# Kernel optimization log

Measured on AMD Instinct MI355X. Metric: run time of the kernel, lower is better.

The kernel has to match this reference:

```python
import jax, jax.numpy as jnp
import numpy as np

B, C, T, H, L = 64, 256, 1536, 512, 2


def setup_inputs() -> dict:
    key = jax.random.key(0)
    ks = jax.random.split(key, 9)
    s = 1.0 / np.sqrt(H)  # PyTorch LSTM init scale
    inp = {
        "x": jax.random.normal(ks[0], (B, C, T), dtype=jnp.float32),
        "Wih0": jax.random.uniform(ks[1], (4 * H, C), jnp.float32, -s, s),
        "Whh0": jax.random.uniform(ks[2], (4 * H, H), jnp.float32, -s, s),
        "bih0": jax.random.uniform(ks[3], (4 * H,), jnp.float32, -s, s),
        "bhh0": jax.random.uniform(ks[4], (4 * H,), jnp.float32, -s, s),
        "Wih1": jax.random.uniform(ks[5], (4 * H, H), jnp.float32, -s, s),
        "Whh1": jax.random.uniform(ks[6], (4 * H, H), jnp.float32, -s, s),
        "bih1": jax.random.uniform(ks[7], (4 * H,), jnp.float32, -s, s),
        "bhh1": jax.random.uniform(ks[8], (4 * H,), jnp.float32, -s, s),
    }
    return inp


def _lstm_layer(x_btf, Wih, Whh, bih, bhh):
    # x_btf: [B, T, F]; gates precomputed from inputs (input GEMM batched over T)
    gx = jnp.einsum("btf,gf->btg", x_btf, Wih) + bih + bhh  # [B, T, 4H]
    gx = jnp.transpose(gx, (1, 0, 2))  # [T, B, 4H] for scan over time
    h0 = jnp.zeros((x_btf.shape[0], H), x_btf.dtype)
    c0 = jnp.zeros_like(h0)

    def step(carry, g_t):
        h, c = carry
        g = g_t + h @ Whh.T  # [B, 4H]
        i, f, gg, o = jnp.split(g, 4, axis=-1)  # PyTorch gate order i,f,g,o
        i = jax.nn.sigmoid(i)
        f = jax.nn.sigmoid(f)
        gg = jnp.tanh(gg)
        o = jax.nn.sigmoid(o)
        c = f * c + i * gg
        h = o * jnp.tanh(c)
        return (h, c), h

    _, hs = jax.lax.scan(step, (h0, c0), gx)  # hs: [T, B, H]
    return jnp.transpose(hs, (1, 0, 2))  # [B, T, H]


def reference(x, Wih0, Whh0, bih0, bhh0, Wih1, Whh1, bih1, bhh1):
    # forward: permute [B, C, T] -> [B, T, C], run 2-layer LSTM, return outputs
    h = jnp.transpose(x, (0, 2, 1))
    h = _lstm_layer(h, Wih0, Whh0, bih0, bhh0)
    h = _lstm_layer(h, Wih1, Whh1, bih1, bhh1)
    return h
```

## Files before the change

kernel.cpp:

```cpp
#include <hip/hip_runtime.h>
#include <cstdint>
#include <cstddef>

#define B_SZ 64
#define T_SZ 1536
#define C_SZ 256
#define H_SZ 512
#define G4H  2048
#define POLL_BUDGET 5000000

typedef __attribute__((ext_vector_type(8))) short short8;
typedef __attribute__((ext_vector_type(4))) float f32x4;

#define AL(p) __hip_atomic_load((p), __ATOMIC_RELAXED, __HIP_MEMORY_SCOPE_AGENT)
#define AS(p, x) __hip_atomic_store((p), (x), __ATOMIC_RELAXED, __HIP_MEMORY_SCOPE_AGENT)
#define SPIN_GE(p, tgt) \
    while (AL(p) < (tgt)) { if (++polls > POLL_BUDGET) break; }

__device__ __forceinline__ unsigned short f2bf_rne(float f) {
    unsigned u = __float_as_uint(f);
    unsigned r = (u + 0x7FFF + ((u >> 16) & 1)) >> 16;
    return (unsigned short)r;
}
__device__ __forceinline__ float sigmoid_f(float x) {
    return 1.f / (1.f + __expf(-x));
}
__device__ __forceinline__ float tanh_f(float x) {
    return 1.f - 2.f / (__expf(2.f * x) + 1.f);
}

template<int AMODE>
__global__ __launch_bounds__(256)
void gemm_gx(const float* __restrict__ A, const float* __restrict__ W,
             const float* __restrict__ bias1, const float* __restrict__ bias2,
             float* __restrict__ gx, int K, int astride_b, int t0g, int tlen)
{
    __shared__ float a_s[8][132];
    __shared__ float b_s[8][132];
    const int tb = blockIdx.x, nb = blockIdx.y, b = blockIdx.z;
    const int tloc = tb * 128;
    const int tglb = t0g + tloc;
    const int r0 = nb * 128;
    const float* Ab = A + (size_t)b * astride_b;
    const int tid = threadIdx.x;
    const int tx = tid & 15, ty = tid >> 4;
    float acc[8][8] = {};

    for (int k0 = 0; k0 < K; k0 += 8) {
        if (AMODE == 0) {
            const int row = tid >> 5;
            const int col = (tid & 31) << 2;
            const float4 v = *(const float4*)(Ab + (size_t)(k0 + row) * T_SZ + tglb + col);
            *(float4*)&a_s[row][col] = v;
        } else {
            const int row  = tid >> 1;
            const int half = (tid & 1) << 2;
            const float4 v = *(const float4*)(Ab + (size_t)(tglb + row) * H_SZ + k0 + half);
            a_s[half + 0][row] = v.x; a_s[half + 1][row] = v.y;
            a_s[half + 2][row] = v.z; a_s[half + 3][row] = v.w;
        }
        {
            const int row  = tid >> 1;
            const int half = (tid & 1) << 2;
            const float4 v = *(const float4*)(W + (size_t)(r0 + row) * K + k0 + half);
            b_s[half + 0][row] = v.x; b_s[half + 1][row] = v.y;
            b_s[half + 2][row] = v.z; b_s[half + 3][row] = v.w;
        }
        __syncthreads();
        #pragma unroll
        for (int kk = 0; kk < 8; ++kk) {
            float4 a0 = *(const float4*)&a_s[kk][tx * 8];
            float4 a1 = *(const float4*)&a_s[kk][tx * 8 + 4];
            float4 w0 = *(const float4*)&b_s[kk][ty * 8];
            float4 w1 = *(const float4*)&b_s[kk][ty * 8 + 4];
            float av[8] = {a0.x, a0.y, a0.z, a0.w, a1.x, a1.y, a1.z, a1.w};
            float wv[8] = {w0.x, w0.y, w0.z, w0.w, w1.x, w1.y, w1.z, w1.w};
            #pragma unroll
            for (int i = 0; i < 8; ++i)
                #pragma unroll
                for (int j = 0; j < 8; ++j)
                    acc[i][j] += wv[i] * av[j];
        }
        __syncthreads();
    }
    float bs[8];
    #pragma unroll
    for (int i = 0; i < 8; ++i)
        bs[i] = bias1[r0 + ty * 8 + i] + bias2[r0 + ty * 8 + i];
    #pragma unroll
    for (int j = 0; j < 8; ++j) {
        float* dst = gx + ((size_t)(tloc + tx * 8 + j) * B_SZ + b) * G4H + r0 + ty * 8;
        float4 o0 = {acc[0][j] + bs[0], acc[1][j] + bs[1], acc[2][j] + bs[2], acc[3][j] + bs[3]};
        float4 o1 = {acc[4][j] + bs[4], acc[5][j] + bs[5], acc[6][j] + bs[6], acc[7][j] + bs[7]};
        *(float4*)dst = o0; *(float4*)(dst + 4) = o1;
    }
}

__global__ void wsplit(const float* __restrict__ w,
                       unsigned short* __restrict__ hi,
                       unsigned short* __restrict__ lo, int n)
{
    const int i = blockIdx.x * 256 + threadIdx.x;
    if (i < n) {
        const float v = w[i];
        const unsigned short h = f2bf_rne(v);
        hi[i] = h;
        lo[i] = f2bf_rne(v - __uint_as_float(((unsigned)h) << 16));
    }
}

__global__ __launch_bounds__(256, 1)
void lstm_fused(const float* __restrict__ gx,
                const unsigned short* __restrict__ w0hi,
                const unsigned short* __restrict__ w0lo,
                const unsigned short* __restrict__ w1ahi,
                const unsigned short* __restrict__ w1alo,
                const unsigned short* __restrict__ w1bhi,
                const unsigned short* __restrict__ w1blo,
                const float* __restrict__ bih1,
                const float* __restrict__ bhh1,
                float* __restrict__ h_out,
                unsigned int* hex0,
                unsigned int* hex1,
                float* __restrict__ c_state,
                unsigned int* prog,
                unsigned int* flag0,
                unsigned int* flag1,
                int t0, int steps, int tlen)
{
    __shared__ __align__(16) char sH0[2][16384];
    __shared__ __align__(16) char sH1[2][16384];

    const int tid  = threadIdx.x;
    const int bid  = blockIdx.x;
    const int role = bid >> 7;
    const int grp  = bid & 3;
    const int w    = (bid >> 2) & 31;
    const int wv   = tid >> 6;
    const int lane = tid & 63;
    const int m16  = lane & 15;
    const int q    = lane >> 4;
    const int ug   = w * 16 + wv * 4 + q;
    const int bg   = grp * 16 + m16;
    const int swz  = (m16 & 7) << 4;

    const int fidx = tid >> 2;
    unsigned int* f0g = flag0 + grp * 128;
    unsigned int* f1g = flag1 + grp * 128;
    const int pidx = w * 4 + wv;

    short8 wahi[16], walo[16];
    short8 wbhi[16], wblo[16];
    {
        const size_t rowbase =
            (size_t)((m16 & 3) * H_SZ + w * 16 + wv * 4 + (m16 >> 2)) * H_SZ + q * 8;
        if (role == 0) {
            #pragma unroll
            for (int kk = 0; kk < 16; ++kk) {
                wahi[kk] = *(const short8*)(w0hi + rowbase + kk * 32);
                walo[kk] = *(const short8*)(w0lo + rowbase + kk * 32);
            }
        } else {
            #pragma unroll
            for (int kk = 0; kk < 16; ++kk) {
                wahi[kk] = *(const short8*)(w1ahi + rowbase + kk * 32);
                walo[kk] = *(const short8*)(w1alo + rowbase + kk * 32);
                wbhi[kk] = *(const short8*)(w1bhi + rowbase + kk * 32);
                wblo[kk] = *(const short8*)(w1blo + rowbase + kk * 32);
            }
        }
    }

    float bsum[4] = {0.f, 0.f, 0.f, 0.f};
    if (role == 1) {
        #pragma unroll
        for (int p = 0; p < 4; ++p)
            bsum[p] = bih1[p * H_SZ + ug] + bhh1[p * H_SZ + ug];
    }

    float c_val = (t0 > 0)
        ? c_state[(size_t)role * B_SZ * H_SZ + (size_t)bg * H_SZ + ug] : 0.f;
    const float* gxp = gx + (size_t)bg * G4H + ug;
    float gxc[4] = {0.f, 0.f, 0.f, 0.f};
    unsigned prview = 0;
    if (role == 0) {
        #pragma unroll
        for (int p = 0; p < 4; ++p) gxc[p] = gxp[p * H_SZ];
        prview = AL(&prog[grp]);
    }
    long long polls = 0;

    for (int tt = 0; tt < steps; ++tt) {
        const int t  = t0 + tt;
        const int pb = tt & 1;
        char* dH0 = sH0[pb];
        char* dH1 = sH1[pb];

        unsigned v0a[16], v0b[16], v1a[16], v1b[16];
        const bool have0 = (role == 1) || (t > 0);
        if (role == 0) {
            if (t > 0) {
                const unsigned tg0 = (unsigned)t;
                const unsigned int* s0 =
                    hex0 + ((size_t)((t - 1) & 7) * 4 + grp) * 8192 + tid;
                #pragma unroll
                for (int m = 0; m < 16; ++m) {
                    v0a[m] = AL(s0 + m * 512);
                    v0b[m] = AL(s0 + m * 512 + 256);
                }
                bool ok = true;
                #pragma unroll
                for (int m = 0; m < 16; ++m)
                    ok &= ((v0a[m] & 0xFFFFu) == tg0) & ((v0b[m] & 0xFFFFu) == tg0);
                if (!ok) {
                    SPIN_GE(f0g + fidx, tg0);
                    SPIN_GE(f0g + fidx + 64, tg0);
                    for (;;) {
                        ok = true;
                        #pragma unroll
                        for (int m = 0; m < 16; ++m) {
                            if ((v0a[m] & 0xFFFFu) != tg0) { v0a[m] = AL(s0 + m * 512); ok = false; }
                            if ((v0b[m] & 0xFFFFu) != tg0) { v0b[m] = AL(s0 + m * 512 + 256); ok = false; }
                        }
                        if (ok || ++polls > POLL_BUDGET) break;
                    }
                }
            }
        } else {
            const unsigned tg0 = (unsigned)(t + 1);
            const unsigned tg1 = (unsigned)t;
            const unsigned int* s0 =
                hex0 + ((size_t)(t & 7) * 4 + grp) * 8192 + tid;
            const unsigned int* s1 =
                hex1 + ((size_t)((t - 1) & 7) * 4 + grp) * 8192 + tid;
            #pragma unroll
            for (int m = 0; m < 16; ++m) {
                v0a[m] = AL(s0 + m * 512);
                v0b[m] = AL(s0 + m * 512 + 256);
            }
            if (t > 0) {
                #pragma unroll
                for (int m = 0; m < 16; ++m) {
                    v1a[m] = AL(s1 + m * 512);
                    v1b[m] = AL(s1 + m * 512 + 256);
                }
            }
            bool ok0 = true;
            #pragma unroll
            for (int m = 0; m < 16; ++m)
                ok0 &= ((v0a[m] & 0xFFFFu) == tg0) & ((v0b[m] & 0xFFFFu) == tg0);
            if (!ok0) {
                SPIN_GE(f0g + fidx, tg0);
                SPIN_GE(f0g + fidx + 64, tg0);
                for (;;) {
                    ok0 = true;
                    #pragma unroll
                    for (int m = 0; m < 16; ++m) {
                        if ((v0a[m] & 0xFFFFu) != tg0) { v0a[m] = AL(s0 + m * 512); ok0 = false; }
                        if ((v0b[m] & 0xFFFFu) != tg0) { v0b[m] = AL(s0 + m * 512 + 256); ok0 = false; }
                    }
                    if (ok0 || ++polls > POLL_BUDGET) break;
                }
            }
            if (t > 0) {
                bool ok1 = true;
                #pragma unroll
                for (int m = 0; m < 16; ++m)
                    ok1 &= ((v1a[m] & 0xFFFFu) == tg1) & ((v1b[m] & 0xFFFFu) == tg1);
                if (!ok1) {
                    SPIN_GE(f1g + fidx, tg1);
                    SPIN_GE(f1g + fidx + 64, tg1);
                    for (;;) {
                        ok1 = true;
                        #pragma unroll
                        for (int m = 0; m < 16; ++m) {
                            if ((v1a[m] & 0xFFFFu) != tg1) { v1a[m] = AL(s1 + m * 512); ok1 = false; }
                            if ((v1b[m] & 0xFFFFu) != tg1) { v1b[m] = AL(s1 + m * 512 + 256); ok1 = false; }
                        }
                        if (ok1 || ++polls > POLL_BUDGET) break;
                    }
                }
            }
            if (w == 0 && tid == 0)
                AS(&prog[grp], (unsigned)(t + 1));
        }
        asm volatile("" ::: "memory");

        if (have0) {
            #pragma unroll
            for (int m = 0; m < 16; ++m) {
                const int oa = ((m << 10) + 2 * tid) ^ ((m & 7) << 4);
                const int ob = ((m << 10) + 2 * (tid + 256)) ^ ((m & 7) << 4);
                *(unsigned short*)(dH0 + oa) = (unsigned short)(v0a[m] >> 16);
                *(unsigned short*)(dH0 + ob) = (unsigned short)(v0b[m] >> 16);
            }
        } else {
            const float4 z = {0.f, 0.f, 0.f, 0.f};
            #pragma unroll
            for (int s = 0; s < 4; ++s)
                *(float4*)(dH0 + tid * 16 + s * 4096) = z;
        }
        if (role == 1) {
            if (t == 0) {
                const float4 z = {0.f, 0.f, 0.f, 0.f};
                #pragma unroll
                for (int s = 0; s < 4; ++s)
                    *(float4*)(dH1 + tid * 16 + s * 4096) = z;
            } else {
                #pragma unroll
                for (int m = 0; m < 16; ++m) {
                    const int oa = ((m << 10) + 2 * tid) ^ ((m & 7) << 4);
                    const int ob = ((m << 10) + 2 * (tid + 256)) ^ ((m & 7) << 4);
                    *(unsigned short*)(dH1 + oa) = (unsigned short)(v1a[m] >> 16);
                    *(unsigned short*)(dH1 + ob) = (unsigned short)(v1b[m] >> 16);
                }
            }
        }
        __syncthreads();

        f32x4 a0 = {0.f, 0.f, 0.f, 0.f};
        f32x4 a2 = {0.f, 0.f, 0.f, 0.f};
        const char* hrec = (role == 0 ? dH0 : dH1) + (m16 << 10);
        const char* hinp = dH0 + (m16 << 10);
        #pragma unroll
        for (int kk = 0; kk < 16; ++kk) {
            const int off = (kk * 64 + q * 16) ^ swz;
            const short8 hr = *(const short8*)(hrec + off);
            a0 = __builtin_amdgcn_mfma_f32_16x16x32_bf16(wahi[kk], hr, a0, 0, 0, 0);
            a2 = __builtin_amdgcn_mfma_f32_16x16x32_bf16(walo[kk], hr, a2, 0, 0, 0);
            if (role == 1) {
                const short8 h0v = *(const short8*)(hinp + off);
                a0 = __builtin_amdgcn_mfma_f32_16x16x32_bf16(wbhi[kk], h0v, a0, 0, 0, 0);
                a2 = __builtin_amdgcn_mfma_f32_16x16x32_bf16(wblo[kk], h0v, a2, 0, 0, 0);
            }
        }

        {
            const float base0 = (role == 0) ? gxc[0] : bsum[0];
            const float base1 = (role == 0) ? gxc[1] : bsum[1];
            const float base2 = (role == 0) ? gxc[2] : bsum[2];
            const float base3 = (role == 0) ? gxc[3] : bsum[3];
            const float si = sigmoid_f(a0[0] + a2[0] + base0);
            const float sf = sigmoid_f(a0[1] + a2[1] + base1);
            const float tc = tanh_f(a0[2] + a2[2] + base2);
            const float so = sigmoid_f(a0[3] + a2[3] + base3);
            c_val = sf * c_val + si * tc;
            const float h = so * tanh_f(c_val);
            const unsigned val = (((unsigned)f2bf_rne(h)) << 16) | (unsigned)(t + 1);
            if (role == 0) {
                while ((int)prview < t - 6) {
                    if (++polls > POLL_BUDGET) break;
                    prview = AL(&prog[grp]);
                }
                AS(hex0 + ((size_t)(t & 7) * 4 + grp) * 8192 + m16 * 512 + ug, val);
                asm volatile("s_waitcnt vmcnt(0)" ::: "memory");
                if (lane == 0) AS(f0g + pidx, (unsigned)(t + 1));
            } else {
                AS(hex1 + ((size_t)(t & 7) * 4 + grp) * 8192 + m16 * 512 + ug, val);
                asm volatile("s_waitcnt vmcnt(0)" ::: "memory");
                if (lane == 0) AS(f1g + pidx, (unsigned)(t + 1));
                h_out[((size_t)bg * T_SZ + t) * H_SZ + ug] = h;
            }
        }
        if (role == 0) {
            if (tt + 1 < steps) {
                const float* gn = gxp + (size_t)(tt + 1) * (B_SZ * G4H);
                #pragma unroll
                for (int p = 0; p < 4; ++p) gxc[p] = gn[p * H_SZ];
            }
            prview = AL(&prog[grp]);
        }
    }
    if (t0 + steps < T_SZ)
        c_state[(size_t)role * B_SZ * H_SZ + (size_t)bg * H_SZ + ug] = c_val;
}

__global__ void debug_ws_beacon(float* out, float v)
{
    if (threadIdx.x == 0 && blockIdx.x == 0) out[0] = v;
}

extern "C" void kernel_launch(void* const* d_in, const int* in_sizes, int n_in,
                              void* d_out, int out_size, void* d_ws, size_t ws_size,
                              hipStream_t stream)
{
    const float* x    = (const float*)d_in[0];
    const float* Wih0 = (const float*)d_in[1];
    const float* Whh0 = (const float*)d_in[2];
    const float* bih0 = (const float*)d_in[3];
    const float* bhh0 = (const float*)d_in[4];
    const float* Wih1 = (const float*)d_in[5];
    const float* Whh1 = (const float*)d_in[6];
    const float* bih1 = (const float*)d_in[7];
    const float* bhh1 = (const float*)d_in[8];
    float* out = (float*)d_out;

    const size_t ringB = (size_t)8 * 4 * 16 * H_SZ * 4;
    const size_t cstB  = (size_t)2 * B_SZ * H_SZ * 4;
    const size_t prgB  = 8192;
    const size_t wB    = (size_t)G4H * H_SZ * 2;
    const size_t fixed = 2 * ringB + cstB + prgB + 6 * wB;

    static const int opts[] = {1536, 768, 512, 384, 256, 128};
    int T_CHUNK = 0;
    for (int i = 0; i < 6; ++i) {
        const size_t need = (size_t)B_SZ * G4H * opts[i] * 4 + fixed;
        if (need <= ws_size) { T_CHUNK = opts[i]; break; }
    }
    if (T_CHUNK == 0) {
        debug_ws_beacon<<<1, 1, 0, stream>>>(out, (float)(ws_size >> 20));
        return;
    }

    char* ws = (char*)d_ws;
    const size_t gxB = (size_t)B_SZ * G4H * T_CHUNK * 4;
    float*          gx      = (float*)ws;
    unsigned int*   hex0    = (unsigned int*)(ws + gxB);
    unsigned int*   hex1    = (unsigned int*)(ws + gxB + ringB);
    float*          c_state = (float*)(ws + gxB + 2 * ringB);
    unsigned int*   prog    = (unsigned int*)(ws + gxB + 2 * ringB + cstB);
    unsigned int*   flag0   = prog + 64;
    unsigned int*   flag1   = flag0 + 512;
    unsigned short* w0hi    = (unsigned short*)(ws + gxB + 2 * ringB + cstB + prgB);
    unsigned short* w0lo    = w0hi  + G4H * H_SZ;
    unsigned short* w1ahi   = w0lo  + G4H * H_SZ;
    unsigned short* w1alo   = w1ahi + G4H * H_SZ;
    unsigned short* w1bhi   = w1alo + G4H * H_SZ;
    unsigned short* w1blo   = w1bhi + G4H * H_SZ;

    const int nW = G4H * H_SZ;
    wsplit<<<(nW + 255) / 256, 256, 0, stream>>>(Whh0, w0hi, w0lo, nW);
    wsplit<<<(nW + 255) / 256, 256, 0, stream>>>(Whh1, w1ahi, w1alo, nW);
    wsplit<<<(nW + 255) / 256, 256, 0, stream>>>(Wih1, w1bhi, w1blo, nW);

    hipMemsetAsync(hex0, 0, 2 * ringB, stream);
    hipMemsetAsync(prog, 0, prgB, stream);

    const dim3 ggrid(T_CHUNK / 128, G4H / 128, B_SZ);
    for (int t0 = 0; t0 < T_SZ; t0 += T_CHUNK) {
        gemm_gx<0><<<ggrid, 256, 0, stream>>>(x, Wih0, bih0, bhh0, gx, C_SZ,
                                              C_SZ * T_SZ, t0, T_CHUNK);
        lstm_fused<<<256, 256, 0, stream>>>(gx, w0hi, w0lo, w1ahi, w1alo,
                                            w1bhi, w1blo, bih1, bhh1, out,
                                            hex0, hex1, c_state, prog,
                                            flag0, flag1, t0, T_CHUNK, T_CHUNK);
    }
}
```

Before: 11.22 ms.

## Halve layer-0 recurrent blocks by giving each two hidden tiles; add spin sleeps

Layer 0 now runs on 64 blocks instead of 128. Each wave holds weights for two groups of 8 hidden units and issues twice the MFMAs per step, so the persistent grid drops from 256 to 192 blocks. Flag polling indices are remapped to match the new producer count. s_sleep is added inside the spin loops to cut memory polling pressure. The trade is a longer per-step critical path on layer 0, double weight registers (risking spills), and possible wake-up latency from the sleeps.

```diff
diff --git a/kernel.cpp b/kernel.cpp
--- a/kernel.cpp
+++ b/kernel.cpp
@@ -15,7 +15,8 @@
 #define AL(p) __hip_atomic_load((p), __ATOMIC_RELAXED, __HIP_MEMORY_SCOPE_AGENT)
 #define AS(p, x) __hip_atomic_store((p), (x), __ATOMIC_RELAXED, __HIP_MEMORY_SCOPE_AGENT)
 #define SPIN_GE(p, tgt) \
-    while (AL(p) < (tgt)) { if (++polls > POLL_BUDGET) break; }
+    while (AL(p) < (tgt)) { __builtin_amdgcn_s_sleep(1); \
+                            if (++polls > POLL_BUDGET) break; }
 
 __device__ __forceinline__ unsigned short f2bf_rne(float f) {
     unsigned u = __float_as_uint(f);
@@ -133,59 +134,73 @@
 
     const int tid  = threadIdx.x;
     const int bid  = blockIdx.x;
-    const int role = bid >> 7;
-    const int grp  = bid & 3;
-    const int w    = (bid >> 2) & 31;
+    const int role = (bid < 64) ? 0 : 1;
+    const int rb   = (role == 0) ? bid : bid - 64;
+    const int grp  = rb & 3;
+    const int w    = rb >> 2;
     const int wv   = tid >> 6;
     const int lane = tid & 63;
     const int m16  = lane & 15;
     const int q    = lane >> 4;
-    const int ug   = w * 16 + wv * 4 + q;
     const int bg   = grp * 16 + m16;
     const int swz  = (m16 & 7) << 4;
 
-    const int fidx = tid >> 2;
+    const int f0A = tid >> 3, f0B = (tid >> 3) + 32;
+    const int f1A = tid >> 2, f1B = (tid >> 2) + 64;
     unsigned int* f0g = flag0 + grp * 128;
     unsigned int* f1g = flag1 + grp * 128;
     const int pidx = w * 4 + wv;
 
-    short8 wahi[16], walo[16];
+    short8 wahi[2][16], walo[2][16];
     short8 wbhi[16], wblo[16];
-    {
+    if (role == 0) {
+        #pragma unroll
+        for (int tau = 0; tau < 2; ++tau) {
+            const size_t rowbase =
+                (size_t)((m16 & 3) * H_SZ + w * 32 + wv * 8 + tau * 4 + (m16 >> 2)) * H_SZ + q * 8;
+            #pragma unroll
+            for (int kk = 0; kk < 16; ++kk) {
+                wahi[tau][kk] = *(const short8*)(w0hi + rowbase + kk * 32);
+                walo[tau][kk] = *(const short8*)(w0lo + rowbase + kk * 32);
+            }
+        }
+    } else {
         const size_t rowbase =
             (size_t)((m16 & 3) * H_SZ + w * 16 + wv * 4 + (m16 >> 2)) * H_SZ + q * 8;
-        if (role == 0) {
-            #pragma unroll
-            for (int kk = 0; kk < 16; ++kk) {
-                wahi[kk] = *(const short8*)(w0hi + rowbase + kk * 32);
-                walo[kk] = *(const short8*)(w0lo + rowbase + kk * 32);
-            }
-        } else {
-            #pragma unroll
-            for (int kk = 0; kk < 16; ++kk) {
-                wahi[kk] = *(const short8*)(w1ahi + rowbase + kk * 32);
-                walo[kk] = *(const short8*)(w1alo + rowbase + kk * 32);
-                wbhi[kk] = *(const short8*)(w1bhi + rowbase + kk * 32);
-                wblo[kk] = *(const short8*)(w1blo + rowbase + kk * 32);
-            }
-        }
-    }
+        #pragma unroll
+        for (int kk = 0; kk < 16; ++kk) {
+            wahi[0][kk] = *(const short8*)(w1ahi + rowbase + kk * 32);
+            walo[0][kk] = *(const short8*)(w1alo + rowbase + kk * 32);
+            wbhi[kk]    = *(const short8*)(w1bhi + rowbase + kk * 32);
+            wblo[kk]    = *(const short8*)(w1blo + rowbase + kk * 32);
+        }
+    }
+
+    const int ugA = (role == 0) ? (w * 32 + wv * 8 + q) : (w * 16 + wv * 4 + q);
+    const int ugB = ugA + 4;
 
     float bsum[4] = {0.f, 0.f, 0.f, 0.f};
     if (role == 1) {
         #pragma unroll
         for (int p = 0; p < 4; ++p)
-            bsum[p] = bih1[p * H_SZ + ug] + bhh1[p * H_SZ + ug];
-    }
-
-    float c_val = (t0 > 0)
-        ? c_state[(size_t)role * B_SZ * H_SZ + (size_t)bg * H_SZ + ug] : 0.f;
-    const float* gxp = gx + (size_t)bg * G4H + ug;
-    float gxc[4] = {0.f, 0.f, 0.f, 0.f};
+            bsum[p] = bih1[p * H_SZ + ugA] + bhh1[p * H_SZ + ugA];
+    }
+
+    float c_valA = 0.f, c_valB = 0.f;
+    if (t0 > 0) {
+        c_valA = c_state[(size_t)role * B_SZ * H_SZ + (size_t)bg * H_SZ + ugA];
+        if (role == 0)
+            c_valB = c_state[(size_t)bg * H_SZ + ugB];
+    }
+    const float* gxp = gx + (size_t)bg * G4H;
+    float gxc[8] = {};
     unsigned prview = 0;
     if (role == 0) {
         #pragma unroll
-        for (int p = 0; p < 4; ++p) gxc[p] = gxp[p * H_SZ];
+        for (int p = 0; p < 4; ++p) {
+            gxc[p]     = gxp[p * H_SZ + ugA];
+            gxc[4 + p] = gxp[p * H_SZ + ugB];
+        }
         prview = AL(&prog[grp]);
     }
     long long polls = 0;
@@ -213,8 +228,8 @@
                 for (int m = 0; m < 16; ++m)
                     ok &= ((v0a[m] & 0xFFFFu) == tg0) & ((v0b[m] & 0xFFFFu) == tg0);
                 if (!ok) {
-                    SPIN_GE(f0g + fidx, tg0);
-                    SPIN_GE(f0g + fidx + 64, tg0);
+                    SPIN_GE(f0g + f0A, tg0);
+                    SPIN_GE(f0g + f0B, tg0);
                     for (;;) {
                         ok = true;
                         #pragma unroll
@@ -250,8 +265,8 @@
             for (int m = 0; m < 16; ++m)
                 ok0 &= ((v0a[m] & 0xFFFFu) == tg0) & ((v0b[m] & 0xFFFFu) == tg0);
             if (!ok0) {
-                SPIN_GE(f0g + fidx, tg0);
-                SPIN_GE(f0g + fidx + 64, tg0);
+                SPIN_GE(f0g + f0A, tg0);
+                SPIN_GE(f0g + f0B, tg0);
                 for (;;) {
                     ok0 = true;
                     #pragma unroll
@@ -268,8 +283,8 @@
                 for (int m = 0; m < 16; ++m)
                     ok1 &= ((v1a[m] & 0xFFFFu) == tg1) & ((v1b[m] & 0xFFFFu) == tg1);
                 if (!ok1) {
-                    SPIN_GE(f1g + fidx, tg1);
-                    SPIN_GE(f1g + fidx + 64, tg1);
+                    SPIN_GE(f1g + f1A, tg1);
+                    SPIN_GE(f1g + f1B, tg1);
                     for (;;) {
                         ok1 = true;
                         #pragma unroll
@@ -318,61 +333,86 @@
         }
         __syncthreads();
 
-        f32x4 a0 = {0.f, 0.f, 0.f, 0.f};
-        f32x4 a2 = {0.f, 0.f, 0.f, 0.f};
-        const char* hrec = (role == 0 ? dH0 : dH1) + (m16 << 10);
-        const char* hinp = dH0 + (m16 << 10);
-        #pragma unroll
-        for (int kk = 0; kk < 16; ++kk) {
-            const int off = (kk * 64 + q * 16) ^ swz;
-            const short8 hr = *(const short8*)(hrec + off);
-            a0 = __builtin_amdgcn_mfma_f32_16x16x32_bf16(wahi[kk], hr, a0, 0, 0, 0);
-            a2 = __builtin_amdgcn_mfma_f32_16x16x32_bf16(walo[kk], hr, a2, 0, 0, 0);
-            if (role == 1) {
+        f32x4 a0A = {0.f, 0.f, 0.f, 0.f}, a2A = {0.f, 0.f, 0.f, 0.f};
+        f32x4 a0B = {0.f, 0.f, 0.f, 0.f}, a2B = {0.f, 0.f, 0.f, 0.f};
+        if (role == 0) {
+            const char* hb = dH0 + (m16 << 10);
+            #pragma unroll
+            for (int kk = 0; kk < 16; ++kk) {
+                const int off = (kk * 64 + q * 16) ^ swz;
+                const short8 hr = *(const short8*)(hb + off);
+                a0A = __builtin_amdgcn_mfma_f32_16x16x32_bf16(wahi[0][kk], hr, a0A, 0, 0, 0);
+                a2A = __builtin_amdgcn_mfma_f32_16x16x32_bf16(walo[0][kk], hr, a2A, 0, 0, 0);
+                a0B = __builtin_amdgcn_mfma_f32_16x16x32_bf16(wahi[1][kk], hr, a0B, 0, 0, 0);
+                a2B = __builtin_amdgcn_mfma_f32_16x16x32_bf16(walo[1][kk], hr, a2B, 0, 0, 0);
+            }
+        } else {
+            const char* hrec = dH1 + (m16 << 10);
+            const char* hinp = dH0 + (m16 << 10);
+            #pragma unroll
+            for (int kk = 0; kk < 16; ++kk) {
+                const int off = (kk * 64 + q * 16) ^ swz;
+                const short8 hr  = *(const short8*)(hrec + off);
                 const short8 h0v = *(const short8*)(hinp + off);
-                a0 = __builtin_amdgcn_mfma_f32_16x16x32_bf16(wbhi[kk], h0v, a0, 0, 0, 0);
-                a2 = __builtin_amdgcn_mfma_f32_16x16x32_bf16(wblo[kk], h0v, a2, 0, 0, 0);
-            }
-        }
-
-        {
-            const float base0 = (role == 0) ? gxc[0] : bsum[0];
-            const float base1 = (role == 0) ? gxc[1] : bsum[1];
-            const float base2 = (role == 0) ? gxc[2] : bsum[2];
-            const float base3 = (role == 0) ? gxc[3] : bsum[3];
-            const float si = sigmoid_f(a0[0] + a2[0] + base0);
-            const float sf = sigmoid_f(a0[1] + a2[1] + base1);
-            const float tc = tanh_f(a0[2] + a2[2] + base2);
-            const float so = sigmoid_f(a0[3] + a2[3] + base3);
-            c_val = sf * c_val + si * tc;
-            const float h = so * tanh_f(c_val);
-            const unsigned val = (((unsigned)f2bf_rne(h)) << 16) | (unsigned)(t + 1);
-            if (role == 0) {
-                while ((int)prview < t - 6) {
-                    if (++polls > POLL_BUDGET) break;
-                    prview = AL(&prog[grp]);
-                }
-                AS(hex0 + ((size_t)(t & 7) * 4 + grp) * 8192 + m16 * 512 + ug, val);
-                asm volatile("s_waitcnt vmcnt(0)" ::: "memory");
-                if (lane == 0) AS(f0g + pidx, (unsigned)(t + 1));
-            } else {
-                AS(hex1 + ((size_t)(t & 7) * 4 + grp) * 8192 + m16 * 512 + ug, val);
-                asm volatile("s_waitcnt vmcnt(0)" ::: "memory");
-                if (lane == 0) AS(f1g + pidx, (unsigned)(t + 1));
-                h_out[((size_t)bg * T_SZ + t) * H_SZ + ug] = h;
-            }
-        }
+                a0A = __builtin_amdgcn_mfma_f32_16x16x32_bf16(wahi[0][kk], hr, a0A, 0, 0, 0);
+                a2A = __builtin_amdgcn_mfma_f32_16x16x32_bf16(walo[0][kk], hr, a2A, 0, 0, 0);
+                a0A = __builtin_amdgcn_mfma_f32_16x16x32_bf16(wbhi[kk], h0v, a0A, 0, 0, 0);
+                a2A = __builtin_amdgcn_mfma_f32_16x16x32_bf16(wblo[kk], h0v, a2A, 0, 0, 0);
+            }
+        }
+
         if (role == 0) {
+            while ((int)prview < t - 6) {
+                __builtin_amdgcn_s_sleep(1);
+                if (++polls > POLL_BUDGET) break;
+                prview = AL(&prog[grp]);
+            }
+            const float siA = sigmoid_f(a0A[0] + a2A[0] + gxc[0]);
+            const float sfA = sigmoid_f(a0A[1] + a2A[1] + gxc[1]);
+            const float tcA = tanh_f(a0A[2] + a2A[2] + gxc[2]);
+            const float soA = sigmoid_f(a0A[3] + a2A[3] + gxc[3]);
+            c_valA = sfA * c_valA + siA * tcA;
+            const float hA = soA * tanh_f(c_valA);
+            const float siB = sigmoid_f(a0B[0] + a2B[0] + gxc[4]);
+            const float sfB = sigmoid_f(a0B[1] + a2B[1] + gxc[5]);
+            const float tcB = tanh_f(a0B[2] + a2B[2] + gxc[6]);
+            const float soB = sigmoid_f(a0B[3] + a2B[3] + gxc[7]);
+            c_valB = sfB * c_valB + siB * tcB;
+            const float hB = soB * tanh_f(c_valB);
+            unsigned int* dst =
+                hex0 + ((size_t)(t & 7) * 4 + grp) * 8192 + m16 * 512;
+            AS(dst + ugA, (((unsigned)f2bf_rne(hA)) << 16) | (unsigned)(t + 1));
+            AS(dst + ugB, (((unsigned)f2bf_rne(hB)) << 16) | (unsigned)(t + 1));
+            asm volatile("s_waitcnt vmcnt(0)" ::: "memory");
+            if (lane == 0) AS(f0g + pidx, (unsigned)(t + 1));
             if (tt + 1 < steps) {
                 const float* gn = gxp + (size_t)(tt + 1) * (B_SZ * G4H);
                 #pragma unroll
-                for (int p = 0; p < 4; ++p) gxc[p] = gn[p * H_SZ];
+                for (int p = 0; p < 4; ++p) {
+                    gxc[p]     = gn[p * H_SZ + ugA];
+                    gxc[4 + p] = gn[p * H_SZ + ugB];
+                }
             }
             prview = AL(&prog[grp]);
-        }
-    }
-    if (t0 + steps < T_SZ)
-        c_state[(size_t)role * B_SZ * H_SZ + (size_t)bg * H_SZ + ug] = c_val;
+        } else {
+            const float si = sigmoid_f(a0A[0] + a2A[0] + bsum[0]);
+            const float sf = sigmoid_f(a0A[1] + a2A[1] + bsum[1]);
+            const float tc = tanh_f(a0A[2] + a2A[2] + bsum[2]);
+            const float so = sigmoid_f(a0A[3] + a2A[3] + bsum[3]);
+            c_valA = sf * c_valA + si * tc;
+            const float h = so * tanh_f(c_valA);
+            AS(hex1 + ((size_t)(t & 7) * 4 + grp) * 8192 + m16 * 512 + ugA,
+               (((unsigned)f2bf_rne(h)) << 16) | (unsigned)(t + 1));
+            asm volatile("s_waitcnt vmcnt(0)" ::: "memory");
+            if (lane == 0) AS(f1g + pidx, (unsigned)(t + 1));
+            h_out[((size_t)bg * T_SZ + t) * H_SZ + ugA] = h;
+        }
+    }
+    if (t0 + steps < T_SZ) {
+        c_state[(size_t)role * B_SZ * H_SZ + (size_t)bg * H_SZ + ugA] = c_valA;
+        if (role == 0)
+            c_state[(size_t)bg * H_SZ + ugB] = c_valB;
+    }
 }
 
 __global__ void debug_ws_beacon(float* out, float v)
@@ -440,7 +480,7 @@
     for (int t0 = 0; t0 < T_SZ; t0 += T_CHUNK) {
         gemm_gx<0><<<ggrid, 256, 0, stream>>>(x, Wih0, bih0, bhh0, gx, C_SZ,
                                               C_SZ * T_SZ, t0, T_CHUNK);
-        lstm_fused<<<256, 256, 0, stream>>>(gx, w0hi, w0lo, w1ahi, w1alo,
+        lstm_fused<<<192, 256, 0, stream>>>(gx, w0hi, w0lo, w1ahi, w1alo,
                                             w1bhi, w1blo, bih1, bhh1, out,
                                             hex0, hex1, c_state, prog,
                                             flag0, flag1, t0, T_CHUNK, T_CHUNK);
```

After: 16.73 ms. +49.1%, slower.
